# Performance work log

Measured on AMD Instinct MI355X. Metric: run time of the kernel, lower is better.

Reference implementation:

```python
import jax, jax.numpy as jnp
import numpy as np

EMBED = 256; M = 8; DV = 32; L = 4; K = 4; SCALE = 0.5
LEVELS = [(128, 128), (64, 64), (32, 32), (16, 16)]  # (H_l, W_l), static
S_TOTAL = sum(h * w for h, w in LEVELS)  # 21760


def _linear_params(key, fan_in, fan_out):
    kw, kb = jax.random.split(key)
    lim = 1.0 / np.sqrt(fan_in)
    W = jax.random.uniform(kw, (fan_in, fan_out), minval=-lim, maxval=lim, dtype=jnp.float32)
    b = jax.random.uniform(kb, (fan_out,), minval=-lim, maxval=lim, dtype=jnp.float32)
    return W, b


def setup_inputs() -> dict:
    key = jax.random.key(0)
    ks = jax.random.split(key, 8)
    N, Q = 2, 8192
    W_off, b_off = _linear_params(ks[0], EMBED, M * L * K * 2)
    W_attn, b_attn = _linear_params(ks[1], EMBED, M * L * K)
    W_val, b_val = _linear_params(ks[2], EMBED, M * DV)
    W_out, b_out = _linear_params(ks[3], M * DV, EMBED)
    queries = jax.random.normal(ks[4], (N, Q, EMBED), dtype=jnp.float32)
    query_geometry_logits = jax.random.normal(ks[5], (N, Q, 4), dtype=jnp.float32)
    value = jax.random.normal(ks[6], (N, S_TOTAL, EMBED), dtype=jnp.float32)
    value_mask = jnp.ones((N, S_TOTAL, 1), dtype=jnp.float32)
    return {"queries": queries, "query_geometry_logits": query_geometry_logits,
            "value": value, "value_mask": value_mask,
            "W_off": W_off, "b_off": b_off, "W_attn": W_attn, "b_attn": b_attn,
            "W_val": W_val, "b_val": b_val, "W_out": W_out, "b_out": b_out}


def _bilinear(img_flat, grid, H, W):
    """grid_sample(mode=bilinear, padding=zeros, align_corners=False).
    img_flat: (B, H*W, C); grid: (B, P, 2) with (x, y) in [-1, 1]."""
    x = (grid[..., 0] + 1.0) * (W * 0.5) - 0.5
    y = (grid[..., 1] + 1.0) * (H * 0.5) - 0.5
    x0f, y0f = jnp.floor(x), jnp.floor(y)
    wx, wy = x - x0f, y - y0f
    x0, y0 = x0f.astype(jnp.int32), y0f.astype(jnp.int32)

    def gather(xi, yi, w):
        valid = (xi >= 0) & (xi < W) & (yi >= 0) & (yi < H)
        idx = jnp.clip(yi, 0, H - 1) * W + jnp.clip(xi, 0, W - 1)
        v = jnp.take_along_axis(img_flat, idx[..., None], axis=1)
        return v * (w * valid)[..., None]

    return (gather(x0, y0, (1 - wx) * (1 - wy)) + gather(x0 + 1, y0, wx * (1 - wy))
            + gather(x0, y0 + 1, (1 - wx) * wy) + gather(x0 + 1, y0 + 1, wx * wy))


def _forward(queries, query_geometry_logits, value, value_mask,
             W_off, b_off, W_attn, b_attn, W_val, b_val, W_out, b_out):
    N, Q, _ = queries.shape
    # attention weights: (N, Q, M, L*K), softmax over the L*K sampling points
    attn = jax.nn.softmax((queries @ W_attn + b_attn).reshape(N, Q, M, L * K), axis=-1)
    # sampling offsets: (N, Q, M, L*K, 2)
    deltas = (queries @ W_off + b_off).reshape(N, Q, M, L * K, 2)
    # reference boxes: sigmoid -> (cx, cy, w, h) in [0, 1]
    b_q = jax.nn.sigmoid(query_geometry_logits)
    xy, wh = b_q[..., :2], b_q[..., 2:]
    scale = wh * (1.0 / K) * SCALE                       # (N, Q, 2)
    pos = xy[:, :, None, None, :] + deltas * scale[:, :, None, None, :]  # (N,Q,M,LK,2)
    # value projection + mask
    v_masked = value_mask * (value @ W_val + b_val)      # (N, S, M*DV)
    # collapse (N, M) for per-head grid sampling
    grid = jnp.clip(2.0 * pos.transpose(0, 2, 1, 3, 4).reshape(N * M, Q, L * K, 2) - 1.0, -1.0, 1.0)
    outs, start = [], 0
    for li, (H, W) in enumerate(LEVELS):
        v_l = v_masked[:, start:start + H * W, :].reshape(N, H * W, M, DV)
        v_l = v_l.transpose(0, 2, 1, 3).reshape(N * M, H * W, DV)
        g_l = grid[:, :, K * li:K * (li + 1), :].reshape(N * M, Q * K, 2)
        s_l = _bilinear(v_l, g_l, H, W)                  # (N*M, Q*K, DV)
        outs.append(s_l.reshape(N, M, Q, K, DV))
        start += H * W
    vals = jnp.concatenate(outs, axis=3)                 # (N, M, Q, L*K, DV)
    vals = vals.transpose(0, 2, 1, 3, 4)                 # (N, Q, M, L*K, DV)
    out = jnp.sum(attn[..., None] * vals, axis=3).reshape(N, Q, M * DV)
    return out @ W_out + b_out                           # (N, Q, EMBED)


def reference(queries, query_geometry_logits, value, value_mask,
              W_off, b_off, W_attn, b_attn, W_val, b_val, W_out, b_out):
    return _forward(queries, query_geometry_logits, value, value_mask,
                    W_off, b_off, W_attn, b_attn, W_val, b_val, W_out, b_out)
```

## Files before the change

### kernel.cpp

```cpp
#include <hip/hip_runtime.h>
#include <math.h>

#define EMBED   256
#define M_HEADS 8
#define DVAL    32
#define LK      16
#define S_TOTAL 21760
#define NQ      8192
#define NROWS   (2 * NQ)
#define QBS     16

typedef __attribute__((ext_vector_type(8))) short s16x8;
typedef __attribute__((ext_vector_type(4))) float f32x4;
typedef unsigned short u16;
typedef unsigned int   u32;

__device__ __forceinline__ short f2bf(float f) {
    unsigned u = __float_as_uint(f);
    u += 0x7fffu + ((u >> 16) & 1u);
    return (short)(u >> 16);
}
__device__ __forceinline__ float bf2f(short h) {
    return __uint_as_float(((unsigned)(u16)h) << 16);
}

#define V_OFF     0
#define V_FLTS    5570560
#define PA_OFF    (V_OFF + V_FLTS)
#define PA_FLTS   6291456
#define MID_OFF   (PA_OFF + PA_FLTS)
#define MID_FLTS  2097152
#define WHI_OFF   (MID_OFF + MID_FLTS)
#define WOA_FLTS  49152
#define WLO_OFF   (WHI_OFF + WOA_FLTS)
#define WV_OFF    (WLO_OFF + WOA_FLTS)
#define WO_OFF    (WV_OFF + 32768)

__global__ __launch_bounds__(256) void prep_kernel(
    const float* __restrict__ W_off, const float* __restrict__ W_attn,
    u16* __restrict__ Whi,           u16* __restrict__ Wlo,
    const float* __restrict__ W_val, u16* __restrict__ Wv,
    const float* __restrict__ W_out, u16* __restrict__ Wo)
{
    const int b = blockIdx.x;
    const int t = threadIdx.x;

    if (b < 512) {
        const int flat = b * 256 + t;
        const int which = flat >> 16;
        const int e = flat & 65535;
        const int k = e >> 8, c = e & 255;
        const float f = which ? W_out[k * 256 + c] : W_val[k * 256 + c];
        const int kt = k >> 5, qd = (k >> 3) & 3, j = k & 7;
        const int idx = (((kt * 256 + c) << 2) + qd) * 8 + j;
        (which ? Wo : Wv)[idx] = (u16)f2bf(f);
    } else {
        const int flat = (b - 512) * 256 + t;
        const int k = flat / 384, c = flat - k * 384;
        const float f = (c < 256) ? W_off[k * 256 + c] : W_attn[k * 128 + (c - 256)];
        const short h = f2bf(f);
        const short lo = f2bf(f - bf2f(h));
        const int kt = k >> 5, qd = (k >> 3) & 3, j = k & 7;
        const int idx = (((kt * 384 + c) << 2) + qd) * 8 + j;
        Whi[idx] = (u16)h;
        Wlo[idx] = (u16)lo;
    }
}

__global__ __launch_bounds__(256, 2) void vproj_kernel(
    const float* __restrict__ value,
    const float* __restrict__ vmask,
    const u16* __restrict__ Wpk,
    const float* __restrict__ b_val,
    u16* __restrict__ v_out)
{
    const int t  = threadIdx.x;
    const int w  = t >> 6, l = t & 63;
    const int c  = l & 15, qd = l >> 4;
    const int r0 = blockIdx.x * 64 + w * 16;

    const float* __restrict__ aptr = value + (size_t)(r0 + c) * EMBED + qd * 8;

    f32x4 acc[16] = {};

    s16x8 bcur[16], bnxt[16];
    float4 a0c, a1c, a0n, a1n;

    a0c = *(const float4*)(aptr);
    a1c = *(const float4*)(aptr + 4);
    #pragma unroll
    for (int nt = 0; nt < 16; ++nt)
        bcur[nt] = *(const s16x8*)(Wpk + (((nt * 16 + c) << 2) + qd) * 8);

    #pragma unroll
    for (int kt = 0; kt < 8; ++kt) {
        if (kt < 7) {
            a0n = *(const float4*)(aptr + (kt + 1) * 32);
            a1n = *(const float4*)(aptr + (kt + 1) * 32 + 4);
            #pragma unroll
            for (int nt = 0; nt < 16; ++nt)
                bnxt[nt] = *(const s16x8*)(Wpk + ((((kt + 1) * 256 + nt * 16 + c) << 2) + qd) * 8);
        }
        const s16x8 a = (s16x8){ f2bf(a0c.x), f2bf(a0c.y), f2bf(a0c.z), f2bf(a0c.w),
                                 f2bf(a1c.x), f2bf(a1c.y), f2bf(a1c.z), f2bf(a1c.w) };
        #pragma unroll
        for (int nt = 0; nt < 16; ++nt)
            acc[nt] = __builtin_amdgcn_mfma_f32_16x16x32_bf16(a, bcur[nt], acc[nt], 0, 0, 0);
        if (kt < 7) {
            a0c = a0n; a1c = a1n;
            #pragma unroll
            for (int nt = 0; nt < 16; ++nt) bcur[nt] = bnxt[nt];
        }
    }

    #pragma unroll
    for (int r = 0; r < 4; ++r) {
        const int grow = r0 + qd * 4 + r;
        const int n = (grow >= S_TOTAL) ? 1 : 0;
        const int s = grow - n * S_TOTAL;
        const float mk = vmask[grow];
        #pragma unroll
        for (int nt = 0; nt < 16; ++nt) {
            const int col = nt * 16 + c;
            const int hm = col >> 5, d = col & 31;
            v_out[((size_t)(n * M_HEADS + hm) * S_TOTAL + s) * DVAL + d] =
                (u16)f2bf((acc[nt][r] + b_val[col]) * mk);
        }
    }
}

__global__ __launch_bounds__(256) void qproj_kernel(
    const float* __restrict__ queries,
    const float* __restrict__ qgl,
    const u16* __restrict__ Whi, const u16* __restrict__ Wlo,
    const float* __restrict__ b_off, const float* __restrict__ b_attn,
    float* __restrict__ pa)
{
    __shared__ float s_off[32][260];
    __shared__ float s_attn[32][132];
    __shared__ float s_geom[32][4];

    const int t  = threadIdx.x;
    const int w  = t >> 6, l = t & 63;
    const int c  = l & 15, qd = l >> 4;
    const int row0 = blockIdx.x * 32;
    const int c0 = w * 96;

    if (t < 32) {
        const float* g = &qgl[(size_t)(row0 + t) * 4];
        s_geom[t][0] = 1.f / (1.f + __expf(-g[0]));
        s_geom[t][1] = 1.f / (1.f + __expf(-g[1]));
        s_geom[t][2] = (1.f / (1.f + __expf(-g[2]))) * 0.125f;
        s_geom[t][3] = (1.f / (1.f + __expf(-g[3]))) * 0.125f;
    }

    f32x4 acc[2][6] = {};

    for (int kt = 0; kt < 8; ++kt) {
        s16x8 ah[2], al[2], bh[6], bl[6];
        #pragma unroll
        for (int mt = 0; mt < 2; ++mt) {
            const float* qp = queries + (size_t)(row0 + mt * 16 + c) * EMBED + kt * 32 + qd * 8;
            const float4 v0 = *(const float4*)qp;
            const float4 v1 = *(const float4*)(qp + 4);
            const short h0 = f2bf(v0.x), h1 = f2bf(v0.y), h2 = f2bf(v0.z), h3 = f2bf(v0.w);
            const short h4 = f2bf(v1.x), h5 = f2bf(v1.y), h6 = f2bf(v1.z), h7 = f2bf(v1.w);
            ah[mt] = (s16x8){ h0, h1, h2, h3, h4, h5, h6, h7 };
            al[mt] = (s16x8){ f2bf(v0.x - bf2f(h0)), f2bf(v0.y - bf2f(h1)),
                              f2bf(v0.z - bf2f(h2)), f2bf(v0.w - bf2f(h3)),
                              f2bf(v1.x - bf2f(h4)), f2bf(v1.y - bf2f(h5)),
                              f2bf(v1.z - bf2f(h6)), f2bf(v1.w - bf2f(h7)) };
        }
        #pragma unroll
        for (int nt = 0; nt < 6; ++nt) {
            const int idx = (((kt * 384 + c0 + nt * 16 + c) << 2) + qd) * 8;
            bh[nt] = *(const s16x8*)(Whi + idx);
            bl[nt] = *(const s16x8*)(Wlo + idx);
        }
        #pragma unroll
        for (int mt = 0; mt < 2; ++mt)
            #pragma unroll
            for (int nt = 0; nt < 6; ++nt) {
                acc[mt][nt] = __builtin_amdgcn_mfma_f32_16x16x32_bf16(ah[mt], bh[nt], acc[mt][nt], 0, 0, 0);
                acc[mt][nt] = __builtin_amdgcn_mfma_f32_16x16x32_bf16(ah[mt], bl[nt], acc[mt][nt], 0, 0, 0);
                acc[mt][nt] = __builtin_amdgcn_mfma_f32_16x16x32_bf16(al[mt], bh[nt], acc[mt][nt], 0, 0, 0);
            }
    }

    #pragma unroll
    for (int mt = 0; mt < 2; ++mt)
        #pragma unroll
        for (int nt = 0; nt < 6; ++nt) {
            const int col = c0 + nt * 16 + c;
            #pragma unroll
            for (int r = 0; r < 4; ++r) {
                const int row = mt * 16 + qd * 4 + r;
                if (col < 256) s_off[row][col] = acc[mt][nt][r] + b_off[col];
                else           s_attn[row][col - 256] = acc[mt][nt][r] + b_attn[col - 256];
            }
        }
    __syncthreads();

    {
        const int qi = t >> 3, hm = t & 7;
        float* a = &s_attn[qi][hm * LK];
        float mx = a[0];
        #pragma unroll
        for (int i = 1; i < LK; ++i) mx = fmaxf(mx, a[i]);
        float s = 0.f;
        #pragma unroll
        for (int i = 0; i < LK; ++i) { const float e = __expf(a[i] - mx); a[i] = e; s += e; }
        const float inv = 1.f / s;
        #pragma unroll
        for (int i = 0; i < LK; ++i) a[i] *= inv;
    }
    __syncthreads();

    for (int p = t; p < 32 * 128; p += 256) {
        const int qi = p >> 7;
        const int pt = p & 127;
        const int lvl = (pt & 15) >> 2;
        const float Wl = (float)(128 >> lvl);
        const float px = fmaf(s_off[qi][2 * pt + 0], s_geom[qi][2], s_geom[qi][0]);
        const float py = fmaf(s_off[qi][2 * pt + 1], s_geom[qi][3], s_geom[qi][1]);
        const float gx = fminf(fmaxf(2.f * px - 1.f, -1.f), 1.f);
        const float gy = fminf(fmaxf(2.f * py - 1.f, -1.f), 1.f);
        const float x = (gx + 1.f) * (Wl * 0.5f) - 0.5f;
        const float y = (gy + 1.f) * (Wl * 0.5f) - 0.5f;
        const size_t idx = ((size_t)(row0 + qi) * 128 + pt) * 3;
        pa[idx + 0] = x;
        pa[idx + 1] = y;
        pa[idx + 2] = s_attn[qi][pt];
    }
}

__global__ __launch_bounds__(256) void sample_kernel(
    const float* __restrict__ pa,
    const u16* __restrict__ v_tab,
    u16* __restrict__ mid)
{
    __shared__ int4   s_idx[QBS * 17];
    __shared__ float4 s_w[QBS * 17];

    const int t    = threadIdx.x;
    const int m    = blockIdx.x & 7;
    const int rest = blockIdx.x >> 3;
    const int qc   = rest & 511;
    const int n    = rest >> 9;
    const int q0   = qc * QBS;

    {
        const int qi = t >> 4, lk = t & 15;
        const int lvl   = lk >> 2;
        const int Wl    = 128 >> lvl;
        const int start = (lvl == 0) ? 0 : (lvl == 1) ? 16384 : (lvl == 2) ? 20480 : 21504;

        const size_t prow = ((size_t)(n * NQ + q0 + qi)) * 128 + m * 16 + lk;
        const float x  = pa[prow * 3 + 0];
        const float y  = pa[prow * 3 + 1];
        const float aw = pa[prow * 3 + 2];

        const float x0f = floorf(x), y0f = floorf(y);
        const int   x0 = (int)x0f, y0 = (int)y0f;
        const float wx = x - x0f, wy = y - y0f;

        const float vx0 = (x0 >= 0) ? 1.f : 0.f;
        const float vx1 = (x0 + 1 <= Wl - 1) ? 1.f : 0.f;
        const float vy0 = (y0 >= 0) ? 1.f : 0.f;
        const float vy1 = (y0 + 1 <= Wl - 1) ? 1.f : 0.f;

        const int xc0 = max(x0, 0);
        const int xc1 = min(x0 + 1, Wl - 1);
        const int yc0 = max(y0, 0);
        const int yc1 = min(y0 + 1, Wl - 1);

        const int e = qi * 17 + lk;
        s_idx[e] = make_int4((start + yc0 * Wl + xc0) * DVAL,
                             (start + yc0 * Wl + xc1) * DVAL,
                             (start + yc1 * Wl + xc0) * DVAL,
                             (start + yc1 * Wl + xc1) * DVAL);
        s_w[e] = make_float4(aw * (1.f - wx) * (1.f - wy) * vx0 * vy0,
                             aw * wx * (1.f - wy) * vx1 * vy0,
                             aw * (1.f - wx) * wy * vx0 * vy1,
                             aw * wx * wy * vx1 * vy1);
    }
    __syncthreads();

    const int g = t >> 4, dp = t & 15;
    const u16* __restrict__ vbp =
        v_tab + (size_t)(n * M_HEADS + m) * S_TOTAL * DVAL + 2 * dp;

    float acc0 = 0.f, acc1 = 0.f;
    #pragma unroll
    for (int lk = 0; lk < LK; ++lk) {
        const int4   id = s_idx[g * 17 + lk];
        const float4 w  = s_w[g * 17 + lk];
        const u32 u0 = *(const u32*)(vbp + id.x);
        const u32 u1 = *(const u32*)(vbp + id.y);
        const u32 u2 = *(const u32*)(vbp + id.z);
        const u32 u3 = *(const u32*)(vbp + id.w);
        acc0 = fmaf(w.x, __uint_as_float(u0 << 16), acc0);
        acc1 = fmaf(w.x, __uint_as_float(u0 & 0xffff0000u), acc1);
        acc0 = fmaf(w.y, __uint_as_float(u1 << 16), acc0);
        acc1 = fmaf(w.y, __uint_as_float(u1 & 0xffff0000u), acc1);
        acc0 = fmaf(w.z, __uint_as_float(u2 << 16), acc0);
        acc1 = fmaf(w.z, __uint_as_float(u2 & 0xffff0000u), acc1);
        acc0 = fmaf(w.w, __uint_as_float(u3 << 16), acc0);
        acc1 = fmaf(w.w, __uint_as_float(u3 & 0xffff0000u), acc1);
    }

    const u32 packed = ((u32)(u16)f2bf(acc1) << 16) | (u32)(u16)f2bf(acc0);
    *(u32*)(mid + ((size_t)(n * NQ + q0 + g)) * EMBED + m * DVAL + 2 * dp) = packed;
}

__global__ __launch_bounds__(256) void out_kernel(
    const u16* __restrict__ mid,
    const u16* __restrict__ Wpk,
    const float* __restrict__ b_out,
    float* __restrict__ out)
{
    const int t  = threadIdx.x;
    const int w  = t >> 6, l = t & 63;
    const int c  = l & 15, qd = l >> 4;
    const int r0 = blockIdx.y * 128 + w * 32;
    const int c0 = blockIdx.x * 64;

    f32x4 acc[2][4] = {};

    for (int kt = 0; kt < 8; ++kt) {
        s16x8 a[2], b[4];
        #pragma unroll
        for (int mt = 0; mt < 2; ++mt)
            a[mt] = *(const s16x8*)(mid + (size_t)(r0 + mt * 16 + c) * EMBED + kt * 32 + qd * 8);
        #pragma unroll
        for (int nt = 0; nt < 4; ++nt)
            b[nt] = *(const s16x8*)(Wpk + (((kt * 256 + c0 + nt * 16 + c) << 2) + qd) * 8);
        #pragma unroll
        for (int mt = 0; mt < 2; ++mt)
            #pragma unroll
            for (int nt = 0; nt < 4; ++nt)
                acc[mt][nt] = __builtin_amdgcn_mfma_f32_16x16x32_bf16(a[mt], b[nt], acc[mt][nt], 0, 0, 0);
    }

    #pragma unroll
    for (int mt = 0; mt < 2; ++mt)
        #pragma unroll
        for (int r = 0; r < 4; ++r) {
            const int row = r0 + mt * 16 + qd * 4 + r;
            #pragma unroll
            for (int nt = 0; nt < 4; ++nt) {
                const int col = c0 + nt * 16 + c;
                out[(size_t)row * EMBED + col] = acc[mt][nt][r] + b_out[col];
            }
        }
}

extern "C" void kernel_launch(void* const* d_in, const int* in_sizes, int n_in,
                              void* d_out, int out_size, void* d_ws, size_t ws_size,
                              hipStream_t stream) {
    (void)in_sizes; (void)n_in; (void)out_size; (void)ws_size;

    const float* queries = (const float*)d_in[0];
    const float* qgl     = (const float*)d_in[1];
    const float* value   = (const float*)d_in[2];
    const float* vmask   = (const float*)d_in[3];
    const float* W_off   = (const float*)d_in[4];
    const float* b_off   = (const float*)d_in[5];
    const float* W_attn  = (const float*)d_in[6];
    const float* b_attn  = (const float*)d_in[7];
    const float* W_val   = (const float*)d_in[8];
    const float* b_val   = (const float*)d_in[9];
    const float* W_out   = (const float*)d_in[10];
    const float* b_out   = (const float*)d_in[11];

    float* ws   = (float*)d_ws;
    u16*  v_ws  = (u16*)(ws + V_OFF);
    float* pa   = ws + PA_OFF;
    u16*  mid   = (u16*)(ws + MID_OFF);
    u16*  whi   = (u16*)(ws + WHI_OFF);
    u16*  wlo   = (u16*)(ws + WLO_OFF);
    u16*  wvpk  = (u16*)(ws + WV_OFF);
    u16*  wopk  = (u16*)(ws + WO_OFF);
    float* outp = (float*)d_out;

    prep_kernel<<<896, 256, 0, stream>>>(W_off, W_attn, whi, wlo,
                                         W_val, wvpk, W_out, wopk);

    vproj_kernel<<<680, 256, 0, stream>>>(value, vmask, wvpk, b_val, v_ws);
    qproj_kernel<<<NROWS / 32, 256, 0, stream>>>(queries, qgl, whi, wlo,
                                                 b_off, b_attn, pa);
    sample_kernel<<<2 * (NQ / QBS) * M_HEADS, 256, 0, stream>>>(pa, v_ws, mid);
    out_kernel<<<dim3(4, 128), 256, 0, stream>>>(mid, wopk, b_out, outp);
}
```

Before: 213.7 us.

## Keep weight tiles register-resident in persistent vproj and out projection kernels

```diff
diff --git a/kernel.cpp b/kernel.cpp
--- a/kernel.cpp
+++ b/kernel.cpp
@@ -77,54 +77,53 @@
     const int t  = threadIdx.x;
     const int w  = t >> 6, l = t & 63;
     const int c  = l & 15, qd = l >> 4;
-    const int r0 = blockIdx.x * 64 + w * 16;
-
-    const float* __restrict__ aptr = value + (size_t)(r0 + c) * EMBED + qd * 8;
-
-    f32x4 acc[16] = {};
-
-    s16x8 bcur[16], bnxt[16];
-    float4 a0c, a1c, a0n, a1n;
-
-    a0c = *(const float4*)(aptr);
-    a1c = *(const float4*)(aptr + 4);
-    #pragma unroll
-    for (int nt = 0; nt < 16; ++nt)
-        bcur[nt] = *(const s16x8*)(Wpk + (((nt * 16 + c) << 2) + qd) * 8);
-
-    #pragma unroll
-    for (int kt = 0; kt < 8; ++kt) {
-        if (kt < 7) {
-            a0n = *(const float4*)(aptr + (kt + 1) * 32);
-            a1n = *(const float4*)(aptr + (kt + 1) * 32 + 4);
-            #pragma unroll
-            for (int nt = 0; nt < 16; ++nt)
-                bnxt[nt] = *(const s16x8*)(Wpk + ((((kt + 1) * 256 + nt * 16 + c) << 2) + qd) * 8);
-        }
-        const s16x8 a = (s16x8){ f2bf(a0c.x), f2bf(a0c.y), f2bf(a0c.z), f2bf(a0c.w),
-                                 f2bf(a1c.x), f2bf(a1c.y), f2bf(a1c.z), f2bf(a1c.w) };
-        #pragma unroll
-        for (int nt = 0; nt < 16; ++nt)
-            acc[nt] = __builtin_amdgcn_mfma_f32_16x16x32_bf16(a, bcur[nt], acc[nt], 0, 0, 0);
-        if (kt < 7) {
-            a0c = a0n; a1c = a1n;
-            #pragma unroll
-            for (int nt = 0; nt < 16; ++nt) bcur[nt] = bnxt[nt];
-        }
-    }
-
-    #pragma unroll
-    for (int r = 0; r < 4; ++r) {
-        const int grow = r0 + qd * 4 + r;
-        const int n = (grow >= S_TOTAL) ? 1 : 0;
-        const int s = grow - n * S_TOTAL;
-        const float mk = vmask[grow];
-        #pragma unroll
-        for (int nt = 0; nt < 16; ++nt) {
-            const int col = nt * 16 + c;
-            const int hm = col >> 5, d = col & 31;
-            v_out[((size_t)(n * M_HEADS + hm) * S_TOTAL + s) * DVAL + d] =
-                (u16)f2bf((acc[nt][r] + b_val[col]) * mk);
+    const int c0 = w * 64;
+
+    s16x8 B[8][4];
+    #pragma unroll
+    for (int kt = 0; kt < 8; ++kt)
+        #pragma unroll
+        for (int nt = 0; nt < 4; ++nt)
+            B[kt][nt] = *(const s16x8*)(Wpk + (((kt * 256 + c0 + nt * 16 + c) << 2) + qd) * 8);
+
+    float bias[4];
+    #pragma unroll
+    for (int nt = 0; nt < 4; ++nt) bias[nt] = b_val[c0 + nt * 16 + c];
+
+    for (int tile = blockIdx.x; tile < 2720; tile += 512) {
+        const int r0 = tile * 16;
+        const float* __restrict__ ap = value + (size_t)(r0 + c) * EMBED + qd * 8;
+
+        float4 a0[8], a1[8];
+        #pragma unroll
+        for (int kt = 0; kt < 8; ++kt) {
+            a0[kt] = *(const float4*)(ap + kt * 32);
+            a1[kt] = *(const float4*)(ap + kt * 32 + 4);
+        }
+
+        f32x4 acc[4] = {};
+        #pragma unroll
+        for (int kt = 0; kt < 8; ++kt) {
+            const s16x8 a = (s16x8){ f2bf(a0[kt].x), f2bf(a0[kt].y), f2bf(a0[kt].z), f2bf(a0[kt].w),
+                                     f2bf(a1[kt].x), f2bf(a1[kt].y), f2bf(a1[kt].z), f2bf(a1[kt].w) };
+            #pragma unroll
+            for (int nt = 0; nt < 4; ++nt)
+                acc[nt] = __builtin_amdgcn_mfma_f32_16x16x32_bf16(a, B[kt][nt], acc[nt], 0, 0, 0);
+        }
+
+        #pragma unroll
+        for (int r = 0; r < 4; ++r) {
+            const int grow = r0 + qd * 4 + r;
+            const int n = (grow >= S_TOTAL) ? 1 : 0;
+            const int s = grow - n * S_TOTAL;
+            const float mk = vmask[grow];
+            #pragma unroll
+            for (int nt = 0; nt < 4; ++nt) {
+                const int col = c0 + nt * 16 + c;
+                const int hm = col >> 5, d = col & 31;
+                v_out[((size_t)(n * M_HEADS + hm) * S_TOTAL + s) * DVAL + d] =
+                    (u16)f2bf((acc[nt][r] + bias[nt]) * mk);
+            }
         }
     }
 }
@@ -313,7 +312,7 @@
     *(u32*)(mid + ((size_t)(n * NQ + q0 + g)) * EMBED + m * DVAL + 2 * dp) = packed;
 }
 
-__global__ __launch_bounds__(256) void out_kernel(
+__global__ __launch_bounds__(256, 2) void out_kernel(
     const u16* __restrict__ mid,
     const u16* __restrict__ Wpk,
     const float* __restrict__ b_out,
@@ -322,37 +321,43 @@
     const int t  = threadIdx.x;
     const int w  = t >> 6, l = t & 63;
     const int c  = l & 15, qd = l >> 4;
-    const int r0 = blockIdx.y * 128 + w * 32;
-    const int c0 = blockIdx.x * 64;
-
-    f32x4 acc[2][4] = {};
-
-    for (int kt = 0; kt < 8; ++kt) {
-        s16x8 a[2], b[4];
-        #pragma unroll
-        for (int mt = 0; mt < 2; ++mt)
-            a[mt] = *(const s16x8*)(mid + (size_t)(r0 + mt * 16 + c) * EMBED + kt * 32 + qd * 8);
+    const int c0 = w * 64;
+
+    s16x8 B[8][4];
+    #pragma unroll
+    for (int kt = 0; kt < 8; ++kt)
         #pragma unroll
         for (int nt = 0; nt < 4; ++nt)
-            b[nt] = *(const s16x8*)(Wpk + (((kt * 256 + c0 + nt * 16 + c) << 2) + qd) * 8);
-        #pragma unroll
-        for (int mt = 0; mt < 2; ++mt)
+            B[kt][nt] = *(const s16x8*)(Wpk + (((kt * 256 + c0 + nt * 16 + c) << 2) + qd) * 8);
+
+    float bias[4];
+    #pragma unroll
+    for (int nt = 0; nt < 4; ++nt) bias[nt] = b_out[c0 + nt * 16 + c];
+
+    for (int tile = blockIdx.x; tile < 1024; tile += 512) {
+        const int r0 = tile * 16;
+        const u16* __restrict__ ap = mid + (size_t)(r0 + c) * EMBED + qd * 8;
+
+        s16x8 a[8];
+        #pragma unroll
+        for (int kt = 0; kt < 8; ++kt)
+            a[kt] = *(const s16x8*)(ap + kt * 32);
+
+        f32x4 acc[4] = {};
+        #pragma unroll
+        for (int kt = 0; kt < 8; ++kt)
             #pragma unroll
             for (int nt = 0; nt < 4; ++nt)
-                acc[mt][nt] = __builtin_amdgcn_mfma_f32_16x16x32_bf16(a[mt], b[nt], acc[mt][nt], 0, 0, 0);
-    }
-
-    #pragma unroll
-    for (int mt = 0; mt < 2; ++mt)
+                acc[nt] = __builtin_amdgcn_mfma_f32_16x16x32_bf16(a[kt], B[kt][nt], acc[nt], 0, 0, 0);
+
         #pragma unroll
         for (int r = 0; r < 4; ++r) {
-            const int row = r0 + mt * 16 + qd * 4 + r;
-            #pragma unroll
-            for (int nt = 0; nt < 4; ++nt) {
-                const int col = c0 + nt * 16 + c;
-                out[(size_t)row * EMBED + col] = acc[mt][nt][r] + b_out[col];
-            }
-        }
+            const int row = r0 + qd * 4 + r;
+            #pragma unroll
+            for (int nt = 0; nt < 4; ++nt)
+                out[(size_t)row * EMBED + c0 + nt * 16 + c] = acc[nt][r] + bias[nt];
+        }
+    }
 }
 
 extern "C" void kernel_launch(void* const* d_in, const int* in_sizes, int n_in,
@@ -386,9 +391,9 @@
     prep_kernel<<<896, 256, 0, stream>>>(W_off, W_attn, whi, wlo,
                                          W_val, wvpk, W_out, wopk);
 
-    vproj_kernel<<<680, 256, 0, stream>>>(value, vmask, wvpk, b_val, v_ws);
+    vproj_kernel<<<512, 256, 0, stream>>>(value, vmask, wvpk, b_val, v_ws);
     qproj_kernel<<<NROWS / 32, 256, 0, stream>>>(queries, qgl, whi, wlo,
                                                  b_off, b_attn, pa);
     sample_kernel<<<2 * (NQ / QBS) * M_HEADS, 256, 0, stream>>>(pa, v_ws, mid);
-    out_kernel<<<dim3(4, 128), 256, 0, stream>>>(mid, wopk, b_out, outp);
-}
+    out_kernel<<<512, 256, 0, stream>>>(mid, wopk, b_out, outp);
+}
```

Result: faster. 205.1 us (-4.0%).
